# Kernel tuning notes

Measured on AMD Instinct MI355X. Metric: run time of the kernel, lower is better.

## Reference

```python
import jax, jax.numpy as jnp
import numpy as np

NUM_USERS = 50000
NUM_ITEMS = 20000
NUM_NODES = NUM_USERS + NUM_ITEMS
FEAT_DIM = 768
HID = 128
NUM_LAYERS = 3
N_EDGES = 2_000_000
LN_EPS = 1e-5


def setup_inputs() -> dict:
    key = jax.random.key(0)
    ks = jax.random.split(key, 12)
    edge_index = jax.random.randint(ks[0], (2, N_EDGES), 0, NUM_NODES, dtype=jnp.int64) if jax.config.jax_enable_x64 else jax.random.randint(ks[0], (2, N_EDGES), 0, NUM_NODES, dtype=jnp.int32)
    item_features = jax.random.normal(ks[1], (NUM_ITEMS, FEAT_DIM), dtype=jnp.float32)
    embedding = jax.random.normal(ks[2], (NUM_NODES, HID), dtype=jnp.float32) * 0.1
    W1 = jax.random.normal(ks[3], (FEAT_DIM, 512), dtype=jnp.float32) * 0.02
    b1 = jnp.zeros((512,), jnp.float32)
    g1 = jnp.ones((512,), jnp.float32)
    be1 = jnp.zeros((512,), jnp.float32)
    W2 = jax.random.normal(ks[4], (512, HID), dtype=jnp.float32) * 0.02
    b2 = jnp.zeros((HID,), jnp.float32)
    g2 = jnp.ones((HID,), jnp.float32)
    be2 = jnp.zeros((HID,), jnp.float32)
    W3 = jax.random.normal(ks[5], (HID, HID), dtype=jnp.float32) * 0.02
    b3 = jnp.zeros((HID,), jnp.float32)
    meta_weight = jnp.asarray(0.01, jnp.float32)
    return {"edge_index": edge_index, "item_features": item_features, "embedding": embedding,
            "W1": W1, "b1": b1, "g1": g1, "be1": be1,
            "W2": W2, "b2": b2, "g2": g2, "be2": be2,
            "W3": W3, "b3": b3, "meta_weight": meta_weight}


def _layer_norm(x, g, b):
    mu = jnp.mean(x, axis=-1, keepdims=True)
    var = jnp.mean(jnp.square(x - mu), axis=-1, keepdims=True)
    return (x - mu) * jax.lax.rsqrt(var + LN_EPS) * g + b


def reference(edge_index, item_features, embedding, W1, b1, g1, be1, W2, b2, g2, be2, W3, b3, meta_weight):
    # item metadata MLP (eval mode: dropout is identity)
    h = jax.nn.relu(_layer_norm(item_features @ W1 + b1, g1, be1))
    h = jax.nn.relu(_layer_norm(h @ W2 + b2, g2, be2))
    h = h @ W3 + b3
    # F.normalize(p=2, dim=-1)
    item_meta = h / jnp.maximum(jnp.linalg.norm(h, axis=-1, keepdims=True), 1e-12)

    # fuse metadata into item id embeddings
    e0 = jnp.concatenate([embedding[:NUM_USERS],
                          embedding[NUM_USERS:] + meta_weight * item_meta], axis=0)

    src, dst = edge_index[0], edge_index[1]
    # symmetric GCN normalization: deg from destination counts
    deg = jax.ops.segment_sum(jnp.ones(src.shape[0], e0.dtype), dst, num_segments=NUM_NODES)
    dinv = jnp.where(deg > 0, jax.lax.rsqrt(jnp.maximum(deg, 1.0)), 0.0)
    norm = (dinv[src] * dinv[dst])[:, None]  # [E, 1]

    alpha = 1.0 / (NUM_LAYERS + 1)
    out = e0 * alpha
    x = e0
    for _ in range(NUM_LAYERS):
        x = jax.ops.segment_sum(x[src] * norm, dst, num_segments=NUM_NODES)
        out = out + x * alpha
    return out
```

## Files before the change

kernel.cpp:

```cpp
#include <hip/hip_runtime.h>
#include <hip/hip_bf16.h>

#define NUM_USERS 50000
#define NUM_ITEMS 20000
#define NUM_NODES (NUM_USERS + NUM_ITEMS)
#define FEAT_DIM 768
#define HID 128
#define H1DIM 512
#define LN_EPS 1e-5f
#define ALPHA 0.25f
#define NBKT 137

typedef __attribute__((ext_vector_type(8))) short short8;
typedef __attribute__((ext_vector_type(4))) float floatx4;

static __device__ inline unsigned short f2bf(float f) {
  unsigned int u = __float_as_uint(f);
  u += 0x7fffu + ((u >> 16) & 1u);
  return (unsigned short)(u >> 16);
}
static __device__ inline float bflo(unsigned int u) {
  return __uint_as_float(u << 16);
}
static __device__ inline float bfhi(unsigned int u) {
  return __uint_as_float(u & 0xffff0000u);
}

__global__ __launch_bounds__(256) void cast_bf16(
    const float* __restrict__ in, unsigned short* __restrict__ out) {
  size_t i = (size_t)blockIdx.x * 256 + threadIdx.x;
  float4 u = ((const float4*)in)[i * 2];
  float4 v = ((const float4*)in)[i * 2 + 1];
  union { unsigned short s[8]; uint4 q; } p;
  p.s[0] = f2bf(u.x); p.s[1] = f2bf(u.y); p.s[2] = f2bf(u.z); p.s[3] = f2bf(u.w);
  p.s[4] = f2bf(v.x); p.s[5] = f2bf(v.y); p.s[6] = f2bf(v.z); p.s[7] = f2bf(v.w);
  ((uint4*)out)[i] = p.q;
}

__global__ __launch_bounds__(256) void transpose_cast(
    const float* __restrict__ W, unsigned short* __restrict__ Wt,
    int K, int N) {
  __shared__ float tile[32][33];
  int tx = threadIdx.x, ty = threadIdx.y;
  int bx = blockIdx.x, by = blockIdx.y;
#pragma unroll
  for (int kk = 0; kk < 4; kk++)
    tile[ty + kk * 8][tx] = W[(size_t)(by * 32 + ty + kk * 8) * N + bx * 32 + tx];
  __syncthreads();
#pragma unroll
  for (int kk = 0; kk < 4; kk++)
    Wt[(size_t)(bx * 32 + ty + kk * 8) * K + by * 32 + tx] =
        f2bf(tile[tx][ty + kk * 8]);
}

__global__ __launch_bounds__(256) void gemm_mfma_bias(
    const unsigned short* __restrict__ A, const unsigned short* __restrict__ Bt,
    const float* __restrict__ bias, float* __restrict__ C,
    int M, int N, int K) {
  __shared__ __align__(16) unsigned short As[128 * 32];
  __shared__ __align__(16) unsigned short Bs[128 * 32];
  const int tid = threadIdx.x;
  const int wave = tid >> 6, lane = tid & 63;
  const int quad = lane >> 4, l16 = lane & 15;
  const int wm = wave >> 1, wn = wave & 1;
  const int bm = blockIdx.y * 128, bn = blockIdx.x * 128;

  floatx4 acc[4][4];
#pragma unroll
  for (int i = 0; i < 4; i++)
#pragma unroll
    for (int j = 0; j < 4; j++) acc[i][j] = (floatx4){0.f, 0.f, 0.f, 0.f};

  const int srow = lane >> 2;
  const int scol = (lane & 3) * 8;

  for (int k0 = 0; k0 < K; k0 += 32) {
#pragma unroll
    for (int i = 0; i < 2; i++) {
      int c = wave * 2 + i;
      int arow = bm + c * 16 + srow;
      if (arow >= M) arow = M - 1;
      const unsigned short* ga = A + (size_t)arow * K + k0 + scol;
      __builtin_amdgcn_global_load_lds(
          (const __attribute__((address_space(1))) unsigned int*)(uintptr_t)ga,
          (__attribute__((address_space(3))) unsigned int*)(uintptr_t)(As + c * 512),
          16, 0, 0);
      int brow = bn + c * 16 + srow;
      const unsigned short* gb = Bt + (size_t)brow * K + k0 + scol;
      __builtin_amdgcn_global_load_lds(
          (const __attribute__((address_space(1))) unsigned int*)(uintptr_t)gb,
          (__attribute__((address_space(3))) unsigned int*)(uintptr_t)(Bs + c * 512),
          16, 0, 0);
    }
    __syncthreads();

    short8 af[4], bf[4];
#pragma unroll
    for (int i = 0; i < 4; i++) {
      af[i] = *(const short8*)&As[(wm * 64 + i * 16 + l16) * 32 + quad * 8];
      bf[i] = *(const short8*)&Bs[(wn * 64 + i * 16 + l16) * 32 + quad * 8];
    }
#pragma unroll
    for (int i = 0; i < 4; i++)
#pragma unroll
      for (int j = 0; j < 4; j++)
        acc[i][j] = __builtin_amdgcn_mfma_f32_16x16x32_bf16(af[i], bf[j],
                                                            acc[i][j], 0, 0, 0);
    __syncthreads();
  }

#pragma unroll
  for (int i = 0; i < 4; i++) {
    int row0 = bm + wm * 64 + i * 16 + quad * 4;
#pragma unroll
    for (int j = 0; j < 4; j++) {
      int col = bn + wn * 64 + j * 16 + l16;
      float bv = bias[col];
#pragma unroll
      for (int r = 0; r < 4; r++) {
        int row = row0 + r;
        if (row < M) C[(size_t)row * N + col] = acc[i][j][r] + bv;
      }
    }
  }
}

__global__ __launch_bounds__(256) void ln_relu_w512_bf16(
    const float* __restrict__ X, const float* __restrict__ g,
    const float* __restrict__ be, unsigned short* __restrict__ O) {
  int row = blockIdx.x, t = threadIdx.x;
  const float* x = X + (size_t)row * H1DIM;
  float v0 = x[t], v1 = x[t + 256];
  float s = v0 + v1, q = v0 * v0 + v1 * v1;
#pragma unroll
  for (int off = 32; off > 0; off >>= 1) {
    s += __shfl_down(s, off);
    q += __shfl_down(q, off);
  }
  __shared__ float ss[4], qq[4];
  int lane = t & 63, wid = t >> 6;
  if (lane == 0) { ss[wid] = s; qq[wid] = q; }
  __syncthreads();
  float S = ss[0] + ss[1] + ss[2] + ss[3];
  float Q = qq[0] + qq[1] + qq[2] + qq[3];
  float mu = S * (1.f / 512.f);
  float var = Q * (1.f / 512.f) - mu * mu;
  float rs = rsqrtf(var + LN_EPS);
  float y0 = (v0 - mu) * rs * g[t] + be[t];
  float y1 = (v1 - mu) * rs * g[t + 256] + be[t + 256];
  unsigned short* o = O + (size_t)row * H1DIM;
  o[t] = f2bf(fmaxf(y0, 0.f));
  o[t + 256] = f2bf(fmaxf(y1, 0.f));
}

__global__ __launch_bounds__(256) void ln_relu_w128(
    float* __restrict__ X, const float* __restrict__ g,
    const float* __restrict__ be, int rows) {
  int gwid = (blockIdx.x * blockDim.x + threadIdx.x) >> 6;
  if (gwid >= rows) return;
  int lane = threadIdx.x & 63;
  float* x = X + (size_t)gwid * HID;
  float v0 = x[lane], v1 = x[lane + 64];
  float s = v0 + v1, q = v0 * v0 + v1 * v1;
#pragma unroll
  for (int off = 32; off > 0; off >>= 1) {
    s += __shfl_down(s, off);
    q += __shfl_down(q, off);
  }
  s = __shfl(s, 0);
  q = __shfl(q, 0);
  float mu = s * (1.f / 128.f);
  float var = q * (1.f / 128.f) - mu * mu;
  float rs = rsqrtf(var + LN_EPS);
  float y0 = (v0 - mu) * rs * g[lane] + be[lane];
  float y1 = (v1 - mu) * rs * g[lane + 64] + be[lane + 64];
  x[lane] = fmaxf(y0, 0.f);
  x[lane + 64] = fmaxf(y1, 0.f);
}

__global__ __launch_bounds__(128) void gemm3_norm4(
    const float* __restrict__ H, const float* __restrict__ W3,
    const float* __restrict__ b3, float* __restrict__ meta) {
  int r0 = blockIdx.x * 4, t = threadIdx.x;
  __shared__ float hrow[4][HID];
#pragma unroll
  for (int r = 0; r < 4; r++) hrow[r][t] = H[(size_t)(r0 + r) * HID + t];
  __syncthreads();
  float s0 = 0.f, s1 = 0.f, s2 = 0.f, s3 = 0.f;
#pragma unroll 4
  for (int k = 0; k < HID; k++) {
    float w = W3[k * HID + t];
    s0 = fmaf(hrow[0][k], w, s0);
    s1 = fmaf(hrow[1][k], w, s1);
    s2 = fmaf(hrow[2][k], w, s2);
    s3 = fmaf(hrow[3][k], w, s3);
  }
  float b = b3[t];
  s0 += b; s1 += b; s2 += b; s3 += b;
  float q0 = s0 * s0, q1 = s1 * s1, q2 = s2 * s2, q3 = s3 * s3;
#pragma unroll
  for (int off = 32; off > 0; off >>= 1) {
    q0 += __shfl_down(q0, off);
    q1 += __shfl_down(q1, off);
    q2 += __shfl_down(q2, off);
    q3 += __shfl_down(q3, off);
  }
  __shared__ float qs[4][2];
  if ((t & 63) == 0) {
    int w = t >> 6;
    qs[0][w] = q0; qs[1][w] = q1; qs[2][w] = q2; qs[3][w] = q3;
  }
  __syncthreads();
  float n0 = fmaxf(sqrtf(qs[0][0] + qs[0][1]), 1e-12f);
  float n1 = fmaxf(sqrtf(qs[1][0] + qs[1][1]), 1e-12f);
  float n2 = fmaxf(sqrtf(qs[2][0] + qs[2][1]), 1e-12f);
  float n3 = fmaxf(sqrtf(qs[3][0] + qs[3][1]), 1e-12f);
  meta[(size_t)(r0 + 0) * HID + t] = s0 / n0;
  meta[(size_t)(r0 + 1) * HID + t] = s1 / n1;
  meta[(size_t)(r0 + 2) * HID + t] = s2 / n2;
  meta[(size_t)(r0 + 3) * HID + t] = s3 / n3;
}

__global__ __launch_bounds__(256) void build_e0_cm2(
    const float* __restrict__ emb, const float* __restrict__ meta,
    const float* __restrict__ mw_p, const float* __restrict__ dinv,
    unsigned int* __restrict__ x0c, float* __restrict__ out) {
  size_t i = (size_t)blockIdx.x * 256 + threadIdx.x;
  int node = (int)(i >> 6);
  int u6 = (int)(i & 63);
  int chunk = u6 >> 5, fl32 = u6 & 31;
  int f0 = chunk * 64 + fl32 * 2;
  float2 e = *(const float2*)&emb[(size_t)node * HID + f0];
  if (node >= NUM_USERS) {
    float2 m = *(const float2*)&meta[(size_t)(node - NUM_USERS) * HID + f0];
    float w = mw_p[0];
    e.x += w * m.x;
    e.y += w * m.y;
  }
  *(float2*)&out[(size_t)node * HID + f0] = make_float2(ALPHA * e.x, ALPHA * e.y);
  float d = dinv[node];
  unsigned pk = (unsigned)f2bf(d * e.x) | ((unsigned)f2bf(d * e.y) << 16);
  x0c[((size_t)chunk * NUM_NODES + node) * 32 + fl32] = pk;
}

__global__ __launch_bounds__(256) void p1_hist(const int* __restrict__ dst,
                                               int* __restrict__ ghist,
                                               int E, int NBL) {
  __shared__ int h[NBKT];
  int t = threadIdx.x;
  if (t < NBKT) h[t] = 0;
  __syncthreads();
  int base = blockIdx.x * 8192;
  for (int i = t; i < 8192; i += 256) {
    int e = base + i;
    if (e < E) atomicAdd(&h[dst[e] >> 9], 1);
  }
  __syncthreads();
  if (t < NBKT) ghist[t * NBL + blockIdx.x] = h[t];
}

__global__ __launch_bounds__(256) void scan_a(const int* __restrict__ in,
                                              int* __restrict__ outp,
                                              int* __restrict__ bsum, int n) {
  int i = blockIdx.x * 256 + threadIdx.x;
  int v = (i < n) ? in[i] : 0;
  int lane = threadIdx.x & 63, wid = threadIdx.x >> 6;
  int s = v;
#pragma unroll
  for (int off = 1; off < 64; off <<= 1) {
    int u = __shfl_up(s, off);
    if (lane >= off) s += u;
  }
  __shared__ int wsum[4];
  if (lane == 63) wsum[wid] = s;
  __syncthreads();
  int add = 0;
  for (int w = 0; w < wid; w++) add += wsum[w];
  int incl = s + add;
  if (i < n) outp[i] = incl - v;
  if (threadIdx.x == 255) bsum[blockIdx.x] = incl;
}

__global__ __launch_bounds__(512) void scan_b(int* __restrict__ bsum, int nb) {
  int t = threadIdx.x;
  int v = (t < nb) ? bsum[t] : 0;
  int lane = t & 63, wid = t >> 6;
  int s = v;
#pragma unroll
  for (int off = 1; off < 64; off <<= 1) {
    int u = __shfl_up(s, off);
    if (lane >= off) s += u;
  }
  __shared__ int ws[8];
  if (lane == 63) ws[wid] = s;
  __syncthreads();
  int add = 0;
  for (int w = 0; w < wid; w++) add += ws[w];
  if (t < nb) bsum[t] = s + add - v;
}

__global__ __launch_bounds__(256) void scan_c(int* __restrict__ outp,
                                              const int* __restrict__ bsum,
                                              int n) {
  int i = blockIdx.x * 256 + threadIdx.x;
  if (i < n) outp[i] += bsum[blockIdx.x];
}

__global__ __launch_bounds__(256) void p1_scatter(
    const int* __restrict__ src, const int* __restrict__ dst,
    const int* __restrict__ gscan, unsigned long long* __restrict__ pairs,
    int E, int NBL) {
  __shared__ int cur[NBKT];
  int t = threadIdx.x;
  if (t < NBKT) cur[t] = gscan[t * NBL + blockIdx.x];
  __syncthreads();
  int base = blockIdx.x * 8192;
  for (int i = t; i < 8192; i += 256) {
    int e = base + i;
    if (e < E) {
      int d = dst[e];
      int pos = atomicAdd(&cur[d >> 9], 1);
      pairs[pos] = ((unsigned long long)(unsigned)d << 32) | (unsigned)src[e];
    }
  }
}

__global__ __launch_bounds__(512) void p2_build(
    const unsigned long long* __restrict__ pairs,
    const int* __restrict__ gscan, int* __restrict__ rowptr,
    int* __restrict__ csr_src, int E, int NBL) {
  __shared__ int hist[512];
  __shared__ int ws8[8];
  int b = blockIdx.x, t = threadIdx.x;
  int base = gscan[b * NBL];
  int end = (b == NBKT - 1) ? E : gscan[(b + 1) * NBL];
  hist[t] = 0;
  __syncthreads();
  for (int i = base + t; i < end; i += 512) {
    unsigned d = (unsigned)(pairs[i] >> 32);
    atomicAdd(&hist[d & 511], 1);
  }
  __syncthreads();
  int v = hist[t];
  int lane = t & 63, wid = t >> 6;
  int s = v;
#pragma unroll
  for (int off = 1; off < 64; off <<= 1) {
    int u = __shfl_up(s, off);
    if (lane >= off) s += u;
  }
  if (lane == 63) ws8[wid] = s;
  __syncthreads();
  int add = 0;
  for (int w = 0; w < wid; w++) add += ws8[w];
  int excl = s + add - v;
  int node = (b << 9) + t;
  if (node < NUM_NODES) rowptr[node] = base + excl;
  if (b == NBKT - 1 && t == 0) rowptr[NUM_NODES] = E;
  __syncthreads();
  hist[t] = base + excl;
  __syncthreads();
  for (int i = base + t; i < end; i += 512) {
    unsigned long long p = pairs[i];
    unsigned d = (unsigned)(p >> 32);
    int pos = atomicAdd(&hist[d & 511], 1);
    csr_src[pos] = (int)(unsigned)p;
  }
}

__global__ __launch_bounds__(256) void calc_dinv2(const int* __restrict__ rowptr,
                                                  float* __restrict__ dinv,
                                                  int n) {
  int i = blockIdx.x * 256 + threadIdx.x;
  if (i < n) {
    int d = rowptr[i + 1] - rowptr[i];
    dinv[i] = d > 0 ? rsqrtf((float)d) : 0.f;
  }
}

#define ACC1(v)                 \
  {                             \
    a0 += bflo((v).x);          \
    a1 += bfhi((v).x);          \
    a2 += bflo((v).y);          \
    a3 += bfhi((v).y);          \
  }

__global__ __launch_bounds__(256) void spmm_chunk2(
    const int* __restrict__ rowptr, const int* __restrict__ csrc,
    const float* __restrict__ dinv, const uint2* __restrict__ xc,
    uint2* __restrict__ yc, float* __restrict__ out, int write_y) {
  int chunk = blockIdx.x & 1;
  int rowblk = blockIdx.x >> 1;
  int tid = threadIdx.x;
  int wave = tid >> 6, lane = tid & 63;
  int slot = lane >> 4, fl = lane & 15;
  int row = rowblk * 16 + wave * 4 + slot;
  bool act = row < NUM_NODES;
  int rr = act ? row : NUM_NODES - 1;
  int beg = rowptr[rr], end = rowptr[rr + 1];
  float wd = dinv[rr];
  const uint2* xq = xc + (size_t)chunk * NUM_NODES * 16 + fl;
  float a0 = 0.f, a1 = 0.f, a2 = 0.f, a3 = 0.f;
  int p = beg;
  int na = (beg + 3) & ~3;
  if (na > end) na = end;
  for (; p < na; p++) {
    int s = csrc[p];
    uint2 v = xq[(size_t)(unsigned)s * 16];
    ACC1(v)
  }
  for (; p + 8 <= end; p += 8) {
    uint4 sA = *(const uint4*)(csrc + p);
    uint4 sB = *(const uint4*)(csrc + p + 4);
    uint2 v0 = xq[(size_t)sA.x * 16];
    uint2 v1 = xq[(size_t)sA.y * 16];
    uint2 v2 = xq[(size_t)sA.z * 16];
    uint2 v3 = xq[(size_t)sA.w * 16];
    uint2 v4 = xq[(size_t)sB.x * 16];
    uint2 v5 = xq[(size_t)sB.y * 16];
    uint2 v6 = xq[(size_t)sB.z * 16];
    uint2 v7 = xq[(size_t)sB.w * 16];
    ACC1(v0) ACC1(v1) ACC1(v2) ACC1(v3)
    ACC1(v4) ACC1(v5) ACC1(v6) ACC1(v7)
  }
  if (p + 4 <= end) {
    uint4 sA = *(const uint4*)(csrc + p);
    uint2 v0 = xq[(size_t)sA.x * 16];
    uint2 v1 = xq[(size_t)sA.y * 16];
    uint2 v2 = xq[(size_t)sA.z * 16];
    uint2 v3 = xq[(size_t)sA.w * 16];
    ACC1(v0) ACC1(v1) ACC1(v2) ACC1(v3)
    p += 4;
  }
  for (; p < end; p++) {
    int s = csrc[p];
    uint2 v = xq[(size_t)(unsigned)s * 16];
    ACC1(v)
  }
  float y0 = wd * a0, y1 = wd * a1, y2 = wd * a2, y3 = wd * a3;
  if (act) {
    if (write_y) {
      unsigned p0 = (unsigned)f2bf(wd * y0) | ((unsigned)f2bf(wd * y1) << 16);
      unsigned p1 = (unsigned)f2bf(wd * y2) | ((unsigned)f2bf(wd * y3) << 16);
      yc[((size_t)chunk * NUM_NODES + row) * 16 + fl] = make_uint2(p0, p1);
    }
    float4* op = (float4*)&out[(size_t)row * HID + chunk * 64 + fl * 4];
    float4 po = *op;
    po.x += ALPHA * y0;
    po.y += ALPHA * y1;
    po.z += ALPHA * y2;
    po.w += ALPHA * y3;
    *op = po;
  }
}

extern "C" void kernel_launch(void* const* d_in, const int* in_sizes, int n_in,
                              void* d_out, int out_size, void* d_ws,
                              size_t ws_size, hipStream_t stream) {
  const int* edge = (const int*)d_in[0];
  const float* item_feat = (const float*)d_in[1];
  const float* emb = (const float*)d_in[2];
  const float* W1 = (const float*)d_in[3];
  const float* b1 = (const float*)d_in[4];
  const float* g1 = (const float*)d_in[5];
  const float* be1 = (const float*)d_in[6];
  const float* W2 = (const float*)d_in[7];
  const float* b2 = (const float*)d_in[8];
  const float* g2 = (const float*)d_in[9];
  const float* be2 = (const float*)d_in[10];
  const float* W3 = (const float*)d_in[11];
  const float* b3 = (const float*)d_in[12];
  const float* mw = (const float*)d_in[13];
  float* out = (float*)d_out;

  const int E = in_sizes[0] / 2;
  const int* src = edge;
  const int* dst = edge + E;
  const int NBL = (E + 8191) / 8192;
  const int nScan = NBKT * NBL;
  const int NBs = (nScan + 255) / 256;

  char* ws = (char*)d_ws;
  float* h1 = (float*)(ws + 0);
  float* h2 = (float*)(ws + 40960000);
  unsigned short* h1b = (unsigned short*)(ws + 51200000);
  uint2* xA = (uint2*)(ws + 51200000);
  unsigned short* Af = (unsigned short*)(ws + 87040000);
  uint2* xB = (uint2*)(ws + 87040000);
  uint2* xC = (uint2*)(ws + 104960000);
  unsigned short* W1t = (unsigned short*)(ws + 122880000);
  unsigned short* W2t = (unsigned short*)(ws + 123666432);
  float* meta = (float*)(ws + 26000000);

  unsigned long long* pairs = (unsigned long long*)(ws + 0);
  int* rowptr = (int*)(ws + 16000000);
  float* dinv = (float*)(ws + 16500000);
  int* ghist = (int*)(ws + 16800000);
  int* gscan = (int*)(ws + 17000000);
  int* bsum = (int*)(ws + 17200000);
  int* csr_src = (int*)(ws + 17500000);

  cast_bf16<<<(NUM_ITEMS * FEAT_DIM / 8) / 256, 256, 0, stream>>>(item_feat, Af);
  transpose_cast<<<dim3(H1DIM / 32, FEAT_DIM / 32), dim3(32, 8), 0, stream>>>(
      W1, W1t, FEAT_DIM, H1DIM);
  transpose_cast<<<dim3(HID / 32, H1DIM / 32), dim3(32, 8), 0, stream>>>(
      W2, W2t, H1DIM, HID);

  gemm_mfma_bias<<<dim3(H1DIM / 128, (NUM_ITEMS + 127) / 128), 256, 0, stream>>>(
      Af, W1t, b1, h1, NUM_ITEMS, H1DIM, FEAT_DIM);
  ln_relu_w512_bf16<<<NUM_ITEMS, 256, 0, stream>>>(h1, g1, be1, h1b);
  gemm_mfma_bias<<<dim3(HID / 128, (NUM_ITEMS + 127) / 128), 256, 0, stream>>>(
      h1b, W2t, b2, h2, NUM_ITEMS, HID, H1DIM);
  ln_relu_w128<<<(NUM_ITEMS * 64) / 256, 256, 0, stream>>>(h2, g2, be2,
                                                           NUM_ITEMS);
  gemm3_norm4<<<NUM_ITEMS / 4, 128, 0, stream>>>(h2, W3, b3, meta);

  p1_hist<<<NBL, 256, 0, stream>>>(dst, ghist, E, NBL);
  scan_a<<<NBs, 256, 0, stream>>>(ghist, gscan, bsum, nScan);
  scan_b<<<1, 512, 0, stream>>>(bsum, NBs);
  scan_c<<<NBs, 256, 0, stream>>>(gscan, bsum, nScan);
  p1_scatter<<<NBL, 256, 0, stream>>>(src, dst, gscan, pairs, E, NBL);
  p2_build<<<NBKT, 512, 0, stream>>>(pairs, gscan, rowptr, csr_src, E, NBL);
  calc_dinv2<<<(NUM_NODES + 255) / 256, 256, 0, stream>>>(rowptr, dinv,
                                                          NUM_NODES);

  build_e0_cm2<<<(NUM_NODES * 64) / 256, 256, 0, stream>>>(
      emb, meta, mw, dinv, (unsigned int*)xA, out);

  const int RG = ((NUM_NODES + 15) / 16) * 2;
  spmm_chunk2<<<RG, 256, 0, stream>>>(rowptr, csr_src, dinv, xA, xB, out, 1);
  spmm_chunk2<<<RG, 256, 0, stream>>>(rowptr, csr_src, dinv, xB, xC, out, 1);
  spmm_chunk2<<<RG, 256, 0, stream>>>(rowptr, csr_src, dinv, xC, nullptr, out, 0);
}
```

Measured before the change: 552.0 us.

## Merge independent MLP and CSR-build stages into shared heterogeneous kernel launches

Independent stages now share a launch by splitting on block index. The weight and feature casts run alongside the destination histogram, GEMM1 alongside the edge scatter, the LN512 alongside the per-bucket CSR build, and GEMM2 alongside the dinv computation. LN128 is folded into the GEMM3 kernel, and edge pairs are packed into 32 bits instead of 64, halving the pair traffic. Together these cut the number of launches and let small graph-preprocessing work fill idle CUs during the MLP. The trade-offs are a reworked workspace layout with overlapping buffers, and the 32-bit packing assumes source ids fit in 17 bits. The LN512 blocks now use 512 threads while only 256 do work.

```diff
diff --git a/kernel.cpp b/kernel.cpp
--- a/kernel.cpp
+++ b/kernel.cpp
@@ -26,44 +26,15 @@
   return __uint_as_float(u & 0xffff0000u);
 }
 
-__global__ __launch_bounds__(256) void cast_bf16(
-    const float* __restrict__ in, unsigned short* __restrict__ out) {
-  size_t i = (size_t)blockIdx.x * 256 + threadIdx.x;
-  float4 u = ((const float4*)in)[i * 2];
-  float4 v = ((const float4*)in)[i * 2 + 1];
-  union { unsigned short s[8]; uint4 q; } p;
-  p.s[0] = f2bf(u.x); p.s[1] = f2bf(u.y); p.s[2] = f2bf(u.z); p.s[3] = f2bf(u.w);
-  p.s[4] = f2bf(v.x); p.s[5] = f2bf(v.y); p.s[6] = f2bf(v.z); p.s[7] = f2bf(v.w);
-  ((uint4*)out)[i] = p.q;
-}
-
-__global__ __launch_bounds__(256) void transpose_cast(
-    const float* __restrict__ W, unsigned short* __restrict__ Wt,
-    int K, int N) {
-  __shared__ float tile[32][33];
-  int tx = threadIdx.x, ty = threadIdx.y;
-  int bx = blockIdx.x, by = blockIdx.y;
-#pragma unroll
-  for (int kk = 0; kk < 4; kk++)
-    tile[ty + kk * 8][tx] = W[(size_t)(by * 32 + ty + kk * 8) * N + bx * 32 + tx];
-  __syncthreads();
-#pragma unroll
-  for (int kk = 0; kk < 4; kk++)
-    Wt[(size_t)(bx * 32 + ty + kk * 8) * K + by * 32 + tx] =
-        f2bf(tile[tx][ty + kk * 8]);
-}
-
-__global__ __launch_bounds__(256) void gemm_mfma_bias(
+static __device__ __forceinline__ void gemm_body(
     const unsigned short* __restrict__ A, const unsigned short* __restrict__ Bt,
-    const float* __restrict__ bias, float* __restrict__ C,
-    int M, int N, int K) {
-  __shared__ __align__(16) unsigned short As[128 * 32];
-  __shared__ __align__(16) unsigned short Bs[128 * 32];
+    const float* __restrict__ bias, float* __restrict__ C, int M, int N, int K,
+    int bx, int by, unsigned short* As, unsigned short* Bs) {
   const int tid = threadIdx.x;
   const int wave = tid >> 6, lane = tid & 63;
   const int quad = lane >> 4, l16 = lane & 15;
   const int wm = wave >> 1, wn = wave & 1;
-  const int bm = blockIdx.y * 128, bn = blockIdx.x * 128;
+  const int bm = by * 128, bn = bx * 128;
 
   floatx4 acc[4][4];
 #pragma unroll
@@ -125,66 +96,261 @@
   }
 }
 
-__global__ __launch_bounds__(256) void ln_relu_w512_bf16(
+#define PREP_CAST_NB 7500
+#define PREP_TW1_NB 384
+#define PREP_TW2_NB 64
+__global__ __launch_bounds__(256) void prep_all(
+    const float* __restrict__ item_feat, unsigned short* __restrict__ Af,
+    const float* __restrict__ W1, unsigned short* __restrict__ W1t,
+    const float* __restrict__ W2, unsigned short* __restrict__ W2t,
+    const int* __restrict__ dst, int* __restrict__ ghist, int E, int NBL) {
+  __shared__ float tile[32][33];
+  __shared__ int h[NBKT];
+  int b = blockIdx.x, t = threadIdx.x;
+  if (b < PREP_CAST_NB) {
+    size_t i = (size_t)b * 256 + t;
+    float4 u = ((const float4*)item_feat)[i * 2];
+    float4 v = ((const float4*)item_feat)[i * 2 + 1];
+    union { unsigned short s[8]; uint4 q; } p;
+    p.s[0] = f2bf(u.x); p.s[1] = f2bf(u.y); p.s[2] = f2bf(u.z); p.s[3] = f2bf(u.w);
+    p.s[4] = f2bf(v.x); p.s[5] = f2bf(v.y); p.s[6] = f2bf(v.z); p.s[7] = f2bf(v.w);
+    ((uint4*)Af)[i] = p.q;
+  } else if (b < PREP_CAST_NB + PREP_TW1_NB + PREP_TW2_NB) {
+    const float* W;
+    unsigned short* Wt;
+    int K, N, bx, by;
+    if (b < PREP_CAST_NB + PREP_TW1_NB) {
+      int tb = b - PREP_CAST_NB;
+      W = W1; Wt = W1t; K = FEAT_DIM; N = H1DIM;
+      bx = tb % (H1DIM / 32); by = tb / (H1DIM / 32);
+    } else {
+      int tb = b - PREP_CAST_NB - PREP_TW1_NB;
+      W = W2; Wt = W2t; K = H1DIM; N = HID;
+      bx = tb % (HID / 32); by = tb / (HID / 32);
+    }
+    int tx = t & 31, ty = t >> 5;
+#pragma unroll
+    for (int kk = 0; kk < 4; kk++)
+      tile[ty + kk * 8][tx] = W[(size_t)(by * 32 + ty + kk * 8) * N + bx * 32 + tx];
+    __syncthreads();
+#pragma unroll
+    for (int kk = 0; kk < 4; kk++)
+      Wt[(size_t)(bx * 32 + ty + kk * 8) * K + by * 32 + tx] =
+          f2bf(tile[tx][ty + kk * 8]);
+  } else {
+    int hb = b - (PREP_CAST_NB + PREP_TW1_NB + PREP_TW2_NB);
+    if (t < NBKT) h[t] = 0;
+    __syncthreads();
+    int base = hb * 8192;
+    for (int i = t; i < 8192; i += 256) {
+      int e = base + i;
+      if (e < E) atomicAdd(&h[dst[e] >> 9], 1);
+    }
+    __syncthreads();
+    if (t < NBKT) ghist[t * NBL + hb] = h[t];
+  }
+}
+
+__global__ __launch_bounds__(256) void scan_a(const int* __restrict__ in,
+                                              int* __restrict__ outp,
+                                              int* __restrict__ bsum, int n) {
+  int i = blockIdx.x * 256 + threadIdx.x;
+  int v = (i < n) ? in[i] : 0;
+  int lane = threadIdx.x & 63, wid = threadIdx.x >> 6;
+  int s = v;
+#pragma unroll
+  for (int off = 1; off < 64; off <<= 1) {
+    int u = __shfl_up(s, off);
+    if (lane >= off) s += u;
+  }
+  __shared__ int wsum[4];
+  if (lane == 63) wsum[wid] = s;
+  __syncthreads();
+  int add = 0;
+  for (int w = 0; w < wid; w++) add += wsum[w];
+  int incl = s + add;
+  if (i < n) outp[i] = incl - v;
+  if (threadIdx.x == 255) bsum[blockIdx.x] = incl;
+}
+
+__global__ __launch_bounds__(512) void scan_b(int* __restrict__ bsum, int nb) {
+  int t = threadIdx.x;
+  int v = (t < nb) ? bsum[t] : 0;
+  int lane = t & 63, wid = t >> 6;
+  int s = v;
+#pragma unroll
+  for (int off = 1; off < 64; off <<= 1) {
+    int u = __shfl_up(s, off);
+    if (lane >= off) s += u;
+  }
+  __shared__ int ws[8];
+  if (lane == 63) ws[wid] = s;
+  __syncthreads();
+  int add = 0;
+  for (int w = 0; w < wid; w++) add += ws[w];
+  if (t < nb) bsum[t] = s + add - v;
+}
+
+__global__ __launch_bounds__(256) void scan_c(int* __restrict__ outp,
+                                              const int* __restrict__ bsum,
+                                              int n) {
+  int i = blockIdx.x * 256 + threadIdx.x;
+  if (i < n) outp[i] += bsum[blockIdx.x];
+}
+
+#define G1_NB 628
+__global__ __launch_bounds__(256) void gemm1_scatter(
+    const unsigned short* __restrict__ Af, const unsigned short* __restrict__ W1t,
+    const float* __restrict__ b1, float* __restrict__ h1,
+    const int* __restrict__ src, const int* __restrict__ dst,
+    const int* __restrict__ gscan, unsigned int* __restrict__ pairs,
+    int E, int NBL) {
+  __shared__ __align__(16) unsigned short As[128 * 32];
+  __shared__ __align__(16) unsigned short Bs[128 * 32];
+  __shared__ int cur[NBKT];
+  int b = blockIdx.x, t = threadIdx.x;
+  if (b < G1_NB) {
+    gemm_body(Af, W1t, b1, h1, NUM_ITEMS, H1DIM, FEAT_DIM, b & 3, b >> 2, As, Bs);
+  } else {
+    int sb = b - G1_NB;
+    if (t < NBKT) cur[t] = gscan[t * NBL + sb];
+    __syncthreads();
+    int base = sb * 8192;
+    for (int i = t; i < 8192; i += 256) {
+      int e = base + i;
+      if (e < E) {
+        int d = dst[e];
+        int pos = atomicAdd(&cur[d >> 9], 1);
+        pairs[pos] = (((unsigned)d & 511u) << 17) | (unsigned)src[e];
+      }
+    }
+  }
+}
+
+__global__ __launch_bounds__(512) void ln512_p2(
+    const unsigned int* __restrict__ pairs, const int* __restrict__ gscan,
+    int* __restrict__ rowptr, int* __restrict__ csr_src, int E, int NBL,
     const float* __restrict__ X, const float* __restrict__ g,
     const float* __restrict__ be, unsigned short* __restrict__ O) {
-  int row = blockIdx.x, t = threadIdx.x;
-  const float* x = X + (size_t)row * H1DIM;
-  float v0 = x[t], v1 = x[t + 256];
-  float s = v0 + v1, q = v0 * v0 + v1 * v1;
-#pragma unroll
-  for (int off = 32; off > 0; off >>= 1) {
-    s += __shfl_down(s, off);
-    q += __shfl_down(q, off);
-  }
+  __shared__ int hist[512];
+  __shared__ int ws8[8];
   __shared__ float ss[4], qq[4];
-  int lane = t & 63, wid = t >> 6;
-  if (lane == 0) { ss[wid] = s; qq[wid] = q; }
-  __syncthreads();
-  float S = ss[0] + ss[1] + ss[2] + ss[3];
-  float Q = qq[0] + qq[1] + qq[2] + qq[3];
-  float mu = S * (1.f / 512.f);
-  float var = Q * (1.f / 512.f) - mu * mu;
-  float rs = rsqrtf(var + LN_EPS);
-  float y0 = (v0 - mu) * rs * g[t] + be[t];
-  float y1 = (v1 - mu) * rs * g[t + 256] + be[t + 256];
-  unsigned short* o = O + (size_t)row * H1DIM;
-  o[t] = f2bf(fmaxf(y0, 0.f));
-  o[t + 256] = f2bf(fmaxf(y1, 0.f));
-}
-
-__global__ __launch_bounds__(256) void ln_relu_w128(
-    float* __restrict__ X, const float* __restrict__ g,
-    const float* __restrict__ be, int rows) {
-  int gwid = (blockIdx.x * blockDim.x + threadIdx.x) >> 6;
-  if (gwid >= rows) return;
-  int lane = threadIdx.x & 63;
-  float* x = X + (size_t)gwid * HID;
-  float v0 = x[lane], v1 = x[lane + 64];
-  float s = v0 + v1, q = v0 * v0 + v1 * v1;
-#pragma unroll
-  for (int off = 32; off > 0; off >>= 1) {
-    s += __shfl_down(s, off);
-    q += __shfl_down(q, off);
-  }
-  s = __shfl(s, 0);
-  q = __shfl(q, 0);
-  float mu = s * (1.f / 128.f);
-  float var = q * (1.f / 128.f) - mu * mu;
-  float rs = rsqrtf(var + LN_EPS);
-  float y0 = (v0 - mu) * rs * g[lane] + be[lane];
-  float y1 = (v1 - mu) * rs * g[lane + 64] + be[lane + 64];
-  x[lane] = fmaxf(y0, 0.f);
-  x[lane + 64] = fmaxf(y1, 0.f);
-}
-
-__global__ __launch_bounds__(128) void gemm3_norm4(
-    const float* __restrict__ H, const float* __restrict__ W3,
+  int b = blockIdx.x, t = threadIdx.x;
+  if (b < NBKT) {
+    int base = gscan[b * NBL];
+    int end = (b == NBKT - 1) ? E : gscan[(b + 1) * NBL];
+    hist[t] = 0;
+    __syncthreads();
+    for (int i = base + t; i < end; i += 512) {
+      unsigned d9 = pairs[i] >> 17;
+      atomicAdd(&hist[d9], 1);
+    }
+    __syncthreads();
+    int v = hist[t];
+    int lane = t & 63, wid = t >> 6;
+    int s = v;
+#pragma unroll
+    for (int off = 1; off < 64; off <<= 1) {
+      int u = __shfl_up(s, off);
+      if (lane >= off) s += u;
+    }
+    if (lane == 63) ws8[wid] = s;
+    __syncthreads();
+    int add = 0;
+    for (int w = 0; w < wid; w++) add += ws8[w];
+    int excl = s + add - v;
+    int node = (b << 9) + t;
+    if (node < NUM_NODES) rowptr[node] = base + excl;
+    if (b == NBKT - 1 && t == 0) rowptr[NUM_NODES] = E;
+    __syncthreads();
+    hist[t] = base + excl;
+    __syncthreads();
+    for (int i = base + t; i < end; i += 512) {
+      unsigned p = pairs[i];
+      int pos = atomicAdd(&hist[p >> 17], 1);
+      csr_src[pos] = (int)(p & 0x1FFFFu);
+    }
+  } else {
+    int row = b - NBKT;
+    const float* x = X + (size_t)row * H1DIM;
+    float v0 = 0.f, v1 = 0.f;
+    int lane = t & 63, wid = t >> 6;
+    if (t < 256) {
+      v0 = x[t];
+      v1 = x[t + 256];
+      float s = v0 + v1, q = v0 * v0 + v1 * v1;
+#pragma unroll
+      for (int off = 32; off > 0; off >>= 1) {
+        s += __shfl_down(s, off);
+        q += __shfl_down(q, off);
+      }
+      if (lane == 0) { ss[wid] = s; qq[wid] = q; }
+    }
+    __syncthreads();
+    if (t < 256) {
+      float S = ss[0] + ss[1] + ss[2] + ss[3];
+      float Q = qq[0] + qq[1] + qq[2] + qq[3];
+      float mu = S * (1.f / 512.f);
+      float var = Q * (1.f / 512.f) - mu * mu;
+      float rs = rsqrtf(var + LN_EPS);
+      float y0 = (v0 - mu) * rs * g[t] + be[t];
+      float y1 = (v1 - mu) * rs * g[t + 256] + be[t + 256];
+      unsigned short* o = O + (size_t)row * H1DIM;
+      o[t] = f2bf(fmaxf(y0, 0.f));
+      o[t + 256] = f2bf(fmaxf(y1, 0.f));
+    }
+  }
+}
+
+#define G2_NB 157
+__global__ __launch_bounds__(256) void gemm2_dinv(
+    const unsigned short* __restrict__ h1b, const unsigned short* __restrict__ W2t,
+    const float* __restrict__ b2, float* __restrict__ h2,
+    const int* __restrict__ rowptr, float* __restrict__ dinv) {
+  __shared__ __align__(16) unsigned short As[128 * 32];
+  __shared__ __align__(16) unsigned short Bs[128 * 32];
+  int b = blockIdx.x, t = threadIdx.x;
+  if (b < G2_NB) {
+    gemm_body(h1b, W2t, b2, h2, NUM_ITEMS, HID, H1DIM, 0, b, As, Bs);
+  } else {
+    int i = (b - G2_NB) * 256 + t;
+    if (i < NUM_NODES) {
+      int d = rowptr[i + 1] - rowptr[i];
+      dinv[i] = d > 0 ? rsqrtf((float)d) : 0.f;
+    }
+  }
+}
+
+__global__ __launch_bounds__(128) void gemm3_fused(
+    const float* __restrict__ H, const float* __restrict__ g2,
+    const float* __restrict__ be2, const float* __restrict__ W3,
     const float* __restrict__ b3, float* __restrict__ meta) {
   int r0 = blockIdx.x * 4, t = threadIdx.x;
   __shared__ float hrow[4][HID];
 #pragma unroll
   for (int r = 0; r < 4; r++) hrow[r][t] = H[(size_t)(r0 + r) * HID + t];
+  __syncthreads();
+  int wv = t >> 6, lane = t & 63;
+#pragma unroll
+  for (int rr = 0; rr < 2; rr++) {
+    int r = wv * 2 + rr;
+    float v0 = hrow[r][lane], v1 = hrow[r][lane + 64];
+    float s = v0 + v1, q = v0 * v0 + v1 * v1;
+#pragma unroll
+    for (int off = 32; off > 0; off >>= 1) {
+      s += __shfl_down(s, off);
+      q += __shfl_down(q, off);
+    }
+    s = __shfl(s, 0);
+    q = __shfl(q, 0);
+    float mu = s * (1.f / 128.f);
+    float var = q * (1.f / 128.f) - mu * mu;
+    float rs = rsqrtf(var + LN_EPS);
+    float y0 = (v0 - mu) * rs * g2[lane] + be2[lane];
+    float y1 = (v1 - mu) * rs * g2[lane + 64] + be2[lane + 64];
+    hrow[r][lane] = fmaxf(y0, 0.f);
+    hrow[r][lane + 64] = fmaxf(y1, 0.f);
+  }
   __syncthreads();
   float s0 = 0.f, s1 = 0.f, s2 = 0.f, s3 = 0.f;
 #pragma unroll 4
@@ -241,141 +407,6 @@
   float d = dinv[node];
   unsigned pk = (unsigned)f2bf(d * e.x) | ((unsigned)f2bf(d * e.y) << 16);
   x0c[((size_t)chunk * NUM_NODES + node) * 32 + fl32] = pk;
-}
-
-__global__ __launch_bounds__(256) void p1_hist(const int* __restrict__ dst,
-                                               int* __restrict__ ghist,
-                                               int E, int NBL) {
-  __shared__ int h[NBKT];
-  int t = threadIdx.x;
-  if (t < NBKT) h[t] = 0;
-  __syncthreads();
-  int base = blockIdx.x * 8192;
-  for (int i = t; i < 8192; i += 256) {
-    int e = base + i;
-    if (e < E) atomicAdd(&h[dst[e] >> 9], 1);
-  }
-  __syncthreads();
-  if (t < NBKT) ghist[t * NBL + blockIdx.x] = h[t];
-}
-
-__global__ __launch_bounds__(256) void scan_a(const int* __restrict__ in,
-                                              int* __restrict__ outp,
-                                              int* __restrict__ bsum, int n) {
-  int i = blockIdx.x * 256 + threadIdx.x;
-  int v = (i < n) ? in[i] : 0;
-  int lane = threadIdx.x & 63, wid = threadIdx.x >> 6;
-  int s = v;
-#pragma unroll
-  for (int off = 1; off < 64; off <<= 1) {
-    int u = __shfl_up(s, off);
-    if (lane >= off) s += u;
-  }
-  __shared__ int wsum[4];
-  if (lane == 63) wsum[wid] = s;
-  __syncthreads();
-  int add = 0;
-  for (int w = 0; w < wid; w++) add += wsum[w];
-  int incl = s + add;
-  if (i < n) outp[i] = incl - v;
-  if (threadIdx.x == 255) bsum[blockIdx.x] = incl;
-}
-
-__global__ __launch_bounds__(512) void scan_b(int* __restrict__ bsum, int nb) {
-  int t = threadIdx.x;
-  int v = (t < nb) ? bsum[t] : 0;
-  int lane = t & 63, wid = t >> 6;
-  int s = v;
-#pragma unroll
-  for (int off = 1; off < 64; off <<= 1) {
-    int u = __shfl_up(s, off);
-    if (lane >= off) s += u;
-  }
-  __shared__ int ws[8];
-  if (lane == 63) ws[wid] = s;
-  __syncthreads();
-  int add = 0;
-  for (int w = 0; w < wid; w++) add += ws[w];
-  if (t < nb) bsum[t] = s + add - v;
-}
-
-__global__ __launch_bounds__(256) void scan_c(int* __restrict__ outp,
-                                              const int* __restrict__ bsum,
-                                              int n) {
-  int i = blockIdx.x * 256 + threadIdx.x;
-  if (i < n) outp[i] += bsum[blockIdx.x];
-}
-
-__global__ __launch_bounds__(256) void p1_scatter(
-    const int* __restrict__ src, const int* __restrict__ dst,
-    const int* __restrict__ gscan, unsigned long long* __restrict__ pairs,
-    int E, int NBL) {
-  __shared__ int cur[NBKT];
-  int t = threadIdx.x;
-  if (t < NBKT) cur[t] = gscan[t * NBL + blockIdx.x];
-  __syncthreads();
-  int base = blockIdx.x * 8192;
-  for (int i = t; i < 8192; i += 256) {
-    int e = base + i;
-    if (e < E) {
-      int d = dst[e];
-      int pos = atomicAdd(&cur[d >> 9], 1);
-      pairs[pos] = ((unsigned long long)(unsigned)d << 32) | (unsigned)src[e];
-    }
-  }
-}
-
-__global__ __launch_bounds__(512) void p2_build(
-    const unsigned long long* __restrict__ pairs,
-    const int* __restrict__ gscan, int* __restrict__ rowptr,
-    int* __restrict__ csr_src, int E, int NBL) {
-  __shared__ int hist[512];
-  __shared__ int ws8[8];
-  int b = blockIdx.x, t = threadIdx.x;
-  int base = gscan[b * NBL];
-  int end = (b == NBKT - 1) ? E : gscan[(b + 1) * NBL];
-  hist[t] = 0;
-  __syncthreads();
-  for (int i = base + t; i < end; i += 512) {
-    unsigned d = (unsigned)(pairs[i] >> 32);
-    atomicAdd(&hist[d & 511], 1);
-  }
-  __syncthreads();
-  int v = hist[t];
-  int lane = t & 63, wid = t >> 6;
-  int s = v;
-#pragma unroll
-  for (int off = 1; off < 64; off <<= 1) {
-    int u = __shfl_up(s, off);
-    if (lane >= off) s += u;
-  }
-  if (lane == 63) ws8[wid] = s;
-  __syncthreads();
-  int add = 0;
-  for (int w = 0; w < wid; w++) add += ws8[w];
-  int excl = s + add - v;
-  int node = (b << 9) + t;
-  if (node < NUM_NODES) rowptr[node] = base + excl;
-  if (b == NBKT - 1 && t == 0) rowptr[NUM_NODES] = E;
-  __syncthreads();
-  hist[t] = base + excl;
-  __syncthreads();
-  for (int i = base + t; i < end; i += 512) {
-    unsigned long long p = pairs[i];
-    unsigned d = (unsigned)(p >> 32);
-    int pos = atomicAdd(&hist[d & 511], 1);
-    csr_src[pos] = (int)(unsigned)p;
-  }
-}
-
-__global__ __launch_bounds__(256) void calc_dinv2(const int* __restrict__ rowptr,
-                                                  float* __restrict__ dinv,
-                                                  int n) {
-  int i = blockIdx.x * 256 + threadIdx.x;
-  if (i < n) {
-    int d = rowptr[i + 1] - rowptr[i];
-    dinv[i] = d > 0 ? rsqrtf((float)d) : 0.f;
-  }
 }
 
 #define ACC1(v)                 \
@@ -483,47 +514,40 @@
 
   char* ws = (char*)d_ws;
   float* h1 = (float*)(ws + 0);
+  float* meta = (float*)(ws + 0);
+  uint2* xB = (uint2*)(ws + 0);
+  uint2* xC = (uint2*)(ws + 18000000);
   float* h2 = (float*)(ws + 40960000);
   unsigned short* h1b = (unsigned short*)(ws + 51200000);
   uint2* xA = (uint2*)(ws + 51200000);
+  unsigned int* pairs = (unsigned int*)(ws + 72000000);
+  int* rowptr = (int*)(ws + 80500000);
+  float* dinv = (float*)(ws + 81000000);
+  int* ghist = (int*)(ws + 81500000);
+  int* gscan = (int*)(ws + 81800000);
+  int* bsum = (int*)(ws + 82100000);
+  int* csr_src = (int*)(ws + 82500000);
   unsigned short* Af = (unsigned short*)(ws + 87040000);
-  uint2* xB = (uint2*)(ws + 87040000);
-  uint2* xC = (uint2*)(ws + 104960000);
   unsigned short* W1t = (unsigned short*)(ws + 122880000);
   unsigned short* W2t = (unsigned short*)(ws + 123666432);
-  float* meta = (float*)(ws + 26000000);
-
-  unsigned long long* pairs = (unsigned long long*)(ws + 0);
-  int* rowptr = (int*)(ws + 16000000);
-  float* dinv = (float*)(ws + 16500000);
-  int* ghist = (int*)(ws + 16800000);
-  int* gscan = (int*)(ws + 17000000);
-  int* bsum = (int*)(ws + 17200000);
-  int* csr_src = (int*)(ws + 17500000);
-
-  cast_bf16<<<(NUM_ITEMS * FEAT_DIM / 8) / 256, 256, 0, stream>>>(item_feat, Af);
-  transpose_cast<<<dim3(H1DIM / 32, FEAT_DIM / 32), dim3(32, 8), 0, stream>>>(
-      W1, W1t, FEAT_DIM, H1DIM);
-  transpose_cast<<<dim3(HID / 32, H1DIM / 32), dim3(32, 8), 0, stream>>>(
-      W2, W2t, H1DIM, HID);
-
-  gemm_mfma_bias<<<dim3(H1DIM / 128, (NUM_ITEMS + 127) / 128), 256, 0, stream>>>(
-      Af, W1t, b1, h1, NUM_ITEMS, H1DIM, FEAT_DIM);
-  ln_relu_w512_bf16<<<NUM_ITEMS, 256, 0, stream>>>(h1, g1, be1, h1b);
-  gemm_mfma_bias<<<dim3(HID / 128, (NUM_ITEMS + 127) / 128), 256, 0, stream>>>(
-      h1b, W2t, b2, h2, NUM_ITEMS, HID, H1DIM);
-  ln_relu_w128<<<(NUM_ITEMS * 64) / 256, 256, 0, stream>>>(h2, g2, be2,
-                                                           NUM_ITEMS);
-  gemm3_norm4<<<NUM_ITEMS / 4, 128, 0, stream>>>(h2, W3, b3, meta);
-
-  p1_hist<<<NBL, 256, 0, stream>>>(dst, ghist, E, NBL);
+
+  prep_all<<<PREP_CAST_NB + PREP_TW1_NB + PREP_TW2_NB + NBL, 256, 0, stream>>>(
+      item_feat, Af, W1, W1t, W2, W2t, dst, ghist, E, NBL);
+
   scan_a<<<NBs, 256, 0, stream>>>(ghist, gscan, bsum, nScan);
   scan_b<<<1, 512, 0, stream>>>(bsum, NBs);
   scan_c<<<NBs, 256, 0, stream>>>(gscan, bsum, nScan);
-  p1_scatter<<<NBL, 256, 0, stream>>>(src, dst, gscan, pairs, E, NBL);
-  p2_build<<<NBKT, 512, 0, stream>>>(pairs, gscan, rowptr, csr_src, E, NBL);
-  calc_dinv2<<<(NUM_NODES + 255) / 256, 256, 0, stream>>>(rowptr, dinv,
-                                                          NUM_NODES);
+
+  gemm1_scatter<<<G1_NB + NBL, 256, 0, stream>>>(Af, W1t, b1, h1, src, dst,
+                                                 gscan, pairs, E, NBL);
+
+  ln512_p2<<<NBKT + NUM_ITEMS, 512, 0, stream>>>(pairs, gscan, rowptr, csr_src,
+                                                 E, NBL, h1, g1, be1, h1b);
+
+  gemm2_dinv<<<G2_NB + (NUM_NODES + 255) / 256, 256, 0, stream>>>(
+      h1b, W2t, b2, h2, rowptr, dinv);
+
+  gemm3_fused<<<NUM_ITEMS / 4, 128, 0, stream>>>(h2, g2, be2, W3, b3, meta);
 
   build_e0_cm2<<<(NUM_NODES * 64) / 256, 256, 0, stream>>>(
       emb, meta, mw, dinv, (unsigned int*)xA, out);
```

Measured after the change: 533.8 us. -3.3%, faster.
